# Performance work log

Measured on AMD Instinct MI355X. Metric: run time of the kernel, lower is better.

## Reference

```python
import jax, jax.numpy as jnp
import numpy as np

LN_EPS = 1e-12


def setup_inputs() -> dict:
    key = jax.random.key(0)
    k1, k2, k3, k4 = jax.random.split(key, 4)
    B, H, L, D = 2, 12, 2048, 64
    q = jax.random.normal(k1, (B, H, L, D), dtype=jnp.float32)
    k = jax.random.normal(k2, (B, H, L, D), dtype=jnp.float32)
    v = jax.random.normal(k3, (B, H, L, D), dtype=jnp.float32)
    mask = jax.random.randint(k4, (1, 1, L, L), 0, 2).astype(jnp.int32)
    gamma = jnp.ones((D,), dtype=jnp.float32)
    beta = jnp.zeros((D,), dtype=jnp.float32)
    return {"q": q, "k": k, "v": v, "mask": mask, "gamma": gamma, "beta": beta}


def reference(q, k, v, mask, gamma, beta):
    # score = q @ k^T  -> [B, H, L, L]
    score = jnp.einsum("bhqd,bhkd->bhqk", q, k)
    # masked_fill(mask == 0, -10000)
    score = jnp.where(mask == 0, jnp.float32(-10000.0), score)
    # result = score @ v -> [B, H, L, D]  (no softmax)
    result = jnp.einsum("bhqk,bhkd->bhqd", score, v)
    # layer norm over the last dim (d_tensor)
    mean = jnp.mean(result, axis=-1, keepdims=True)
    var = jnp.var(result, axis=-1, keepdims=True)
    normed = (result - mean) / jnp.sqrt(var + LN_EPS)
    return normed * gamma + beta
```

## Files before the change

### kernel.cpp

```cpp
#include <hip/hip_runtime.h>

#define SEQ 2048
#define HD 64
#define NBH 24

#define MB_OFF   0
#define MB_BYTES (32 * 32 * 512)
#define QB_OFF   (MB_OFF + MB_BYTES)
#define QK_BYTES (NBH * SEQ * HD * 2)
#define KB_OFF   (QB_OFF + QK_BYTES)
#define VT_OFF   (KB_OFF + QK_BYTES)
#define WS_NEED  ((size_t)(VT_OFF + QK_BYTES))

typedef __bf16 bfrag8 __attribute__((ext_vector_type(8)));
typedef __bf16 bf16x4 __attribute__((ext_vector_type(4)));
typedef float  floatx4 __attribute__((ext_vector_type(4)));
typedef float  floatx16 __attribute__((ext_vector_type(16)));

__device__ __forceinline__ floatx4 mfma_16x16x32(bfrag8 a, bfrag8 b, floatx4 c) {
    return __builtin_amdgcn_mfma_f32_16x16x32_bf16(a, b, c, 0, 0, 0);
}
__device__ __forceinline__ floatx16 mfma_32x32x16(bfrag8 a, bfrag8 b, floatx16 c) {
    return __builtin_amdgcn_mfma_f32_32x32x16_bf16(a, b, c, 0, 0, 0);
}
__device__ __forceinline__ void gld16(const unsigned char* g, unsigned char* l) {
    __builtin_amdgcn_global_load_lds(
        (const __attribute__((address_space(1))) unsigned int*)g,
        (__attribute__((address_space(3))) unsigned int*)l, 16, 0, 0);
}

__global__ __launch_bounds__(256)
void prep_kernel(const float* __restrict__ qp, const float* __restrict__ kp,
                 const float* __restrict__ vp, const int* __restrict__ maskp,
                 unsigned char* __restrict__ ws)
{
    __shared__ __attribute__((aligned(16))) unsigned char parena[64 * 68 * 4];
    const int t = threadIdx.x;
    const int b = blockIdx.x;

    if (b < 1536) {
        int gt  = b * 256 + t;
        int row = gt >> 3;
        int c   = gt & 7;
        const floatx4* qs = (const floatx4*)(qp + row * 64 + c * 8);
        const floatx4* ks = (const floatx4*)(kp + row * 64 + c * 8);
        floatx4 q0 = qs[0], q1 = qs[1];
        floatx4 k0 = ks[0], k1 = ks[1];
        bfrag8 qpk, kpk;
        #pragma unroll
        for (int i = 0; i < 4; ++i) {
            qpk[i] = (__bf16)q0[i]; qpk[4 + i] = (__bf16)q1[i];
            kpk[i] = (__bf16)k0[i]; kpk[4 + i] = (__bf16)k1[i];
        }
        *(bfrag8*)(ws + QB_OFF + row * 128 + c * 16) = qpk;
        *(bfrag8*)(ws + KB_OFF + row * 128 + ((c ^ (row & 7)) * 16)) = kpk;
    } else if (b < 2304) {
        int bb = b - 1536, bh = bb >> 5, kt = bb & 31;
        float* lf = (float*)parena;
        const floatx4* vg = (const floatx4*)(vp + (bh * SEQ + kt * 64) * 64);
        #pragma unroll
        for (int it = 0; it < 4; ++it) {
            int f = t + it * 256;
            int r = f >> 4, c4 = f & 15;
            floatx4 val = vg[f];
            #pragma unroll
            for (int i = 0; i < 4; ++i) lf[r * 68 + c4 * 4 + i] = val[i];
        }
        __syncthreads();
        int d = t >> 2, kseg = t & 3;
        unsigned char* tb = ws + VT_OFF + (size_t)(bh * 32 + kt) * 8192 + d * 128;
        #pragma unroll
        for (int jj = 0; jj < 2; ++jj) {
            bfrag8 pk;
            #pragma unroll
            for (int e = 0; e < 8; ++e)
                pk[e] = (__bf16)lf[(kseg * 16 + jj * 8 + e) * 68 + d];
            *(bfrag8*)(tb + (((kseg * 2 + jj) ^ (d & 7)) * 16)) = pk;
        }
    } else {
        int cc = b - 2304, qtb = cc >> 5, kt = cc & 31;
        const int w = t >> 6, lane = t & 63;
        #pragma unroll
        for (int it = 0; it < 16; ++it) {
            int rr = it * 4 + w;
            unsigned long long bl = __ballot(maskp[(qtb * 64 + rr) * SEQ + kt * 64 + lane] != 0);
            if (lane == 0)
                *(unsigned long long*)(ws + MB_OFF + (size_t)((qtb * 32 + kt) * 64 + rr) * 8) = bl;
        }
    }
}

__global__ __launch_bounds__(256, 2)
void normattn_main(const unsigned char* __restrict__ ws,
                   const float* __restrict__ gammap, const float* __restrict__ betap,
                   float* __restrict__ outp)
{
    __shared__ __attribute__((aligned(16))) unsigned char sm[65536];

    const int tid  = threadIdx.x;
    const int w    = tid >> 6;
    const int lane = tid & 63;
    const int l32  = lane & 31;
    const int hi   = lane >> 5;

    const int id   = blockIdx.x;
    const int xcd  = id & 7;
    const int s    = id >> 3;
    const int bh   = xcd * 3 + (s >> 5);
    const int qtb  = s & 31;
    const int q0   = qtb * 64;

    unsigned char* slotK = sm + w * 16384;
    unsigned char* slotV = slotK + 8192;

    const unsigned char* gKt = ws + KB_OFF + (size_t)(bh * SEQ) * 128;
    const unsigned char* gVt = ws + VT_OFF + (size_t)(bh * 32) * 8192;
    const unsigned char* gMb = ws + MB_OFF + (size_t)(qtb * 32) * 512;

    bfrag8 qb[2][4];
    #pragma unroll
    for (int qh = 0; qh < 2; ++qh)
        #pragma unroll
        for (int dstep = 0; dstep < 4; ++dstep)
            qb[qh][dstep] = *(const bfrag8*)(ws + QB_OFF +
                (size_t)(bh * SEQ + q0 + qh * 32 + l32) * 128 + dstep * 32 + hi * 16);

    floatx16 acc[2][2];
    #pragma unroll
    for (int i = 0; i < 4; ++i) acc[i >> 1][i & 1] = (floatx16)0.0f;

    auto stage = [&](int kt) {
        const unsigned char* gk = gKt + (size_t)kt * 8192 + lane * 16;
        const unsigned char* gv = gVt + (size_t)kt * 8192 + lane * 16;
        #pragma unroll
        for (int c = 0; c < 8; ++c) {
            gld16(gk + c * 1024, slotK + c * 1024);
            gld16(gv + c * 1024, slotV + c * 1024);
        }
    };
    unsigned long long mnx0, mnx1;
    auto loadmask = [&](int kt) {
        mnx0 = *(const unsigned long long*)(gMb + (size_t)kt * 512 + l32 * 8);
        mnx1 = *(const unsigned long long*)(gMb + (size_t)kt * 512 + 256 + l32 * 8);
    };

    stage(w);
    loadmask(w);

    for (int i = 0; i < 8; ++i) {
        const int kt = w + 4 * i;
        asm volatile("s_waitcnt vmcnt(0)" ::: "memory");
        const unsigned long long mr0 = mnx0, mr1 = mnx1;

        bfrag8 ka[2][4], va[2][2][2];
        #pragma unroll
        for (int kh = 0; kh < 2; ++kh)
            #pragma unroll
            for (int d = 0; d < 4; ++d)
                ka[kh][d] = *(const bfrag8*)(slotK + (kh * 32 + l32) * 128 +
                                             (((d * 2 + hi) ^ (l32 & 7)) << 4));
        #pragma unroll
        for (int dh = 0; dh < 2; ++dh)
            #pragma unroll
            for (int kh = 0; kh < 2; ++kh)
                #pragma unroll
                for (int ks = 0; ks < 2; ++ks)
                    va[dh][kh][ks] = *(const bfrag8*)(slotV + (dh * 32 + l32) * 128 +
                                                      (((kh * 4 + ks * 2 + hi) ^ (l32 & 7)) << 4));
        asm volatile("s_waitcnt lgkmcnt(0)" ::: "memory");
        if (i < 7) { stage(kt + 4); loadmask(kt + 4); }

        #pragma unroll
        for (int kh = 0; kh < 2; ++kh) {
            floatx16 st0 = (floatx16)0.0f, st1 = (floatx16)0.0f;
            #pragma unroll
            for (int d = 0; d < 4; ++d) {
                st0 = mfma_32x32x16(ka[kh][d], qb[0][d], st0);
                st1 = mfma_32x32x16(ka[kh][d], qb[1][d], st1);
            }
            #pragma unroll
            for (int qh = 0; qh < 2; ++qh) {
                const floatx16 st = qh ? st1 : st0;
                const unsigned long long mrow = qh ? mr1 : mr0;
                const unsigned bits = (unsigned)(mrow >> (kh * 32 + 4 * hi));
                unsigned u[8];
                #pragma unroll
                for (int j = 0; j < 8; ++j) {
                    const int kl0 = 2 * (j & 1) + 8 * (j >> 1);
                    float a = ((bits >> kl0) & 1u) ? st[2 * j] : -10000.0f;
                    float b = ((bits >> (kl0 + 1)) & 1u) ? st[2 * j + 1] : -10000.0f;
                    asm("v_cvt_pk_bf16_f32 %0, %1, %2" : "=v"(u[j]) : "v"(a), "v"(b));
                }
                asm("v_permlane32_swap_b32 %0, %1" : "+v"(u[0]), "+v"(u[2]));
                asm("v_permlane32_swap_b32 %0, %1" : "+v"(u[1]), "+v"(u[3]));
                asm("v_permlane32_swap_b32 %0, %1" : "+v"(u[4]), "+v"(u[6]));
                asm("v_permlane32_swap_b32 %0, %1" : "+v"(u[5]), "+v"(u[7]));
                union { unsigned int w4[4]; bfrag8 f; } c0, c1;
                c0.w4[0] = u[0]; c0.w4[1] = u[1]; c0.w4[2] = u[2]; c0.w4[3] = u[3];
                c1.w4[0] = u[4]; c1.w4[1] = u[5]; c1.w4[2] = u[6]; c1.w4[3] = u[7];

                acc[qh][0] = mfma_32x32x16(va[0][kh][0], c0.f, acc[qh][0]);
                acc[qh][0] = mfma_32x32x16(va[0][kh][1], c1.f, acc[qh][0]);
                acc[qh][1] = mfma_32x32x16(va[1][kh][0], c0.f, acc[qh][1]);
                acc[qh][1] = mfma_32x32x16(va[1][kh][1], c1.f, acc[qh][1]);
            }
        }
    }

    #pragma unroll
    for (int qh = 0; qh < 2; ++qh)
        #pragma unroll
        for (int dh = 0; dh < 2; ++dh)
            #pragma unroll
            for (int jj = 0; jj < 4; ++jj) {
                floatx4 t;
                #pragma unroll
                for (int e = 0; e < 4; ++e) t[e] = acc[qh][dh][jj * 4 + e];
                *(floatx4*)(sm + w * 16384 + (qh * 2 + dh) * 4096 + jj * 1024 + lane * 16) = t;
            }
    __syncthreads();
    if (w < 2) {
        const int qh = w;
        floatx16 o2[2];
        #pragma unroll
        for (int dh = 0; dh < 2; ++dh)
            #pragma unroll
            for (int jj = 0; jj < 4; ++jj) {
                floatx4 s4 = (floatx4)0.0f;
                #pragma unroll
                for (int ww = 0; ww < 4; ++ww) {
                    floatx4 t = *(const floatx4*)(sm + ww * 16384 + (qh * 2 + dh) * 4096 +
                                                  jj * 1024 + lane * 16);
                    #pragma unroll
                    for (int e = 0; e < 4; ++e) s4[e] += t[e];
                }
                #pragma unroll
                for (int e = 0; e < 4; ++e) o2[dh][jj * 4 + e] = s4[e];
            }
        float ss = 0.0f, ss2 = 0.0f;
        #pragma unroll
        for (int dh = 0; dh < 2; ++dh)
            #pragma unroll
            for (int r = 0; r < 16; ++r) { float x = o2[dh][r]; ss += x; ss2 += x * x; }
        ss  += __shfl_xor(ss, 32);
        ss2 += __shfl_xor(ss2, 32);
        float mean = ss * (1.0f / 64.0f);
        float var  = ss2 * (1.0f / 64.0f) - mean * mean;
        float rstd = rsqrtf(var + 1e-12f);
        float* orow = outp + (size_t)(bh * SEQ + q0 + qh * 32 + l32) * 64;
        #pragma unroll
        for (int dh = 0; dh < 2; ++dh)
            #pragma unroll
            for (int jj = 0; jj < 4; ++jj) {
                const int d0 = dh * 32 + jj * 8 + 4 * hi;
                floatx4 gg = *(const floatx4*)(gammap + d0);
                floatx4 bb = *(const floatx4*)(betap + d0);
                floatx4 o;
                #pragma unroll
                for (int e = 0; e < 4; ++e)
                    o[e] = (o2[dh][jj * 4 + e] - mean) * rstd * gg[e] + bb[e];
                *(floatx4*)(orow + d0) = o;
            }
    }
}

#define KROW 72
#define SROW 40
__global__ __launch_bounds__(256, 4)
void normattn_fallback(const float* __restrict__ qp, const float* __restrict__ kp,
                       const float* __restrict__ vp, const int* __restrict__ maskp,
                       const float* __restrict__ gammap, const float* __restrict__ betap,
                       float* __restrict__ outp)
{
    __shared__ __attribute__((aligned(16))) __bf16 sQ[64 * KROW];
    __shared__ __attribute__((aligned(16))) __bf16 sK[64 * KROW];
    __shared__ __attribute__((aligned(16))) __bf16 sV[64 * KROW];
    __shared__ __attribute__((aligned(16))) __bf16 sS[4][16 * SROW];
    __shared__ __attribute__((aligned(8)))  unsigned int sMw[64][2];

    const int tid = threadIdx.x, wave = tid >> 6, lane = tid & 63;
    const int quad = lane >> 4, l16 = lane & 15;
    const int q0 = blockIdx.x * 64, bh = blockIdx.y;
    const int base = bh * SEQ * HD;
    {
        const floatx4* qg = (const floatx4*)(qp + base + q0 * HD);
        #pragma unroll
        for (int it = 0; it < 4; ++it) {
            int idx = tid + it * 256, r = idx >> 4, c = idx & 15;
            floatx4 val = qg[idx];
            bf16x4 pk = {(__bf16)val[0], (__bf16)val[1], (__bf16)val[2], (__bf16)val[3]};
            *(bf16x4*)&sQ[r * KROW + c * 4] = pk;
        }
    }
    __syncthreads();
    bfrag8 qa0 = *(const bfrag8*)&sQ[(wave * 16 + l16) * KROW + quad * 8];
    bfrag8 qa1 = *(const bfrag8*)&sQ[(wave * 16 + l16) * KROW + quad * 8 + 32];
    floatx4 acc[4];
    #pragma unroll
    for (int i = 0; i < 4; ++i) acc[i] = (floatx4)0.0f;
    const int qrow_loc = wave * 16 + quad * 4;
    const int qrb = q0 + qrow_loc;
    for (int kb = 0; kb < SEQ; kb += 64) {
        __syncthreads();
        {
            const floatx4* kg = (const floatx4*)(kp + base + kb * HD);
            #pragma unroll
            for (int it = 0; it < 4; ++it) {
                int idx = tid + it * 256, r = idx >> 4, c = idx & 15;
                floatx4 val = kg[idx];
                bf16x4 pk = {(__bf16)val[0], (__bf16)val[1], (__bf16)val[2], (__bf16)val[3]};
                *(bf16x4*)&sK[r * KROW + c * 4] = pk;
            }
        }
        {
            int d = tid & 63;
            #pragma unroll
            for (int it = 0; it < 4; ++it) {
                int k4 = (tid >> 6) + it * 4;
                bf16x4 pk;
                #pragma unroll
                for (int i = 0; i < 4; ++i) pk[i] = (__bf16)vp[base + (kb + k4 * 4 + i) * HD + d];
                *(bf16x4*)&sV[d * KROW + k4 * 4] = pk;
            }
        }
        #pragma unroll
        for (int it = 0; it < 16; ++it) {
            int rr = it * 4 + wave;
            unsigned long long bl = __ballot(maskp[(q0 + rr) * SEQ + kb + lane] != 0);
            if (lane == 0) { sMw[rr][0] = (unsigned)bl; sMw[rr][1] = (unsigned)(bl >> 32); }
        }
        __syncthreads();
        unsigned long long mrow[4];
        #pragma unroll
        for (int r = 0; r < 4; ++r) mrow[r] = *(const unsigned long long*)&sMw[qrow_loc + r][0];
        #pragma unroll
        for (int kc = 0; kc < 64; kc += 32) {
            floatx4 s0 = (floatx4)0.0f, s1 = (floatx4)0.0f;
            bfrag8 b00 = *(const bfrag8*)&sK[(kc + l16) * KROW + quad * 8];
            bfrag8 b01 = *(const bfrag8*)&sK[(kc + l16) * KROW + quad * 8 + 32];
            bfrag8 b10 = *(const bfrag8*)&sK[(kc + 16 + l16) * KROW + quad * 8];
            bfrag8 b11 = *(const bfrag8*)&sK[(kc + 16 + l16) * KROW + quad * 8 + 32];
            s0 = mfma_16x16x32(qa0, b00, s0);
            s0 = mfma_16x16x32(qa1, b01, s0);
            s1 = mfma_16x16x32(qa0, b10, s1);
            s1 = mfma_16x16x32(qa1, b11, s1);
            #pragma unroll
            for (int r = 0; r < 4; ++r) {
                float v0 = ((mrow[r] >> (kc + l16)) & 1ull) ? s0[r] : -10000.0f;
                float v1 = ((mrow[r] >> (kc + 16 + l16)) & 1ull) ? s1[r] : -10000.0f;
                sS[wave][(quad * 4 + r) * SROW + l16] = (__bf16)v0;
                sS[wave][(quad * 4 + r) * SROW + 16 + l16] = (__bf16)v1;
            }
            asm volatile("s_waitcnt lgkmcnt(0)" ::: "memory");
            bfrag8 pa = *(const bfrag8*)&sS[wave][l16 * SROW + quad * 8];
            #pragma unroll
            for (int nt = 0; nt < 4; ++nt) {
                bfrag8 vb = *(const bfrag8*)&sV[(nt * 16 + l16) * KROW + kc + quad * 8];
                acc[nt] = mfma_16x16x32(pa, vb, acc[nt]);
            }
        }
    }
    float g[4], bt[4];
    #pragma unroll
    for (int nt = 0; nt < 4; ++nt) { g[nt] = gammap[nt * 16 + l16]; bt[nt] = betap[nt * 16 + l16]; }
    #pragma unroll
    for (int r = 0; r < 4; ++r) {
        float s = 0.0f, s2 = 0.0f;
        #pragma unroll
        for (int nt = 0; nt < 4; ++nt) { float xx = acc[nt][r]; s += xx; s2 += xx * xx; }
        #pragma unroll
        for (int off = 1; off < 16; off <<= 1) { s += __shfl_xor(s, off); s2 += __shfl_xor(s2, off); }
        float mean = s * (1.0f / 64.0f);
        float var = s2 * (1.0f / 64.0f) - mean * mean;
        float rstd = rsqrtf(var + 1e-12f);
        float* orow = outp + base + (qrb + r) * HD;
        #pragma unroll
        for (int nt = 0; nt < 4; ++nt)
            orow[nt * 16 + l16] = (acc[nt][r] - mean) * rstd * g[nt] + bt[nt];
    }
}

extern "C" void kernel_launch(void* const* d_in, const int* in_sizes, int n_in,
                              void* d_out, int out_size, void* d_ws, size_t ws_size,
                              hipStream_t stream) {
    const float* q     = (const float*)d_in[0];
    const float* k     = (const float*)d_in[1];
    const float* v     = (const float*)d_in[2];
    const int*   mask  = (const int*)d_in[3];
    const float* gamma = (const float*)d_in[4];
    const float* beta  = (const float*)d_in[5];
    float* out = (float*)d_out;

    if (ws_size >= WS_NEED) {
        unsigned char* ws = (unsigned char*)d_ws;
        prep_kernel<<<3328, 256, 0, stream>>>(q, k, v, mask, ws);
        normattn_main<<<768, 256, 0, stream>>>(ws, gamma, beta, out);
    } else {
        dim3 grid(32, NBH);
        normattn_fallback<<<grid, 256, 0, stream>>>(q, k, v, mask, gamma, beta, out);
    }
}
```

Measured before the change: 135.4 us.

## Process 128 query rows per block with Q staged in swizzled LDS

Measured after the change: 141.0 us. +4.1%, slower.

```diff
diff --git a/kernel.cpp b/kernel.cpp
--- a/kernel.cpp
+++ b/kernel.cpp
@@ -52,7 +52,7 @@
             qpk[i] = (__bf16)q0[i]; qpk[4 + i] = (__bf16)q1[i];
             kpk[i] = (__bf16)k0[i]; kpk[4 + i] = (__bf16)k1[i];
         }
-        *(bfrag8*)(ws + QB_OFF + row * 128 + c * 16) = qpk;
+        *(bfrag8*)(ws + QB_OFF + row * 128 + ((c ^ (row & 7)) * 16)) = qpk;
         *(bfrag8*)(ws + KB_OFF + row * 128 + ((c ^ (row & 7)) * 16)) = kpk;
     } else if (b < 2304) {
         int bb = b - 1536, bh = bb >> 5, kt = bb & 31;
@@ -95,7 +95,7 @@
                    const float* __restrict__ gammap, const float* __restrict__ betap,
                    float* __restrict__ outp)
 {
-    __shared__ __attribute__((aligned(16))) unsigned char sm[65536];
+    __shared__ __attribute__((aligned(16))) unsigned char sm[81920];
 
     const int tid  = threadIdx.x;
     const int w    = tid >> 6;
@@ -106,161 +106,200 @@
     const int id   = blockIdx.x;
     const int xcd  = id & 7;
     const int s    = id >> 3;
-    const int bh   = xcd * 3 + (s >> 5);
-    const int qtb  = s & 31;
-    const int q0   = qtb * 64;
+    const int bh   = xcd * 3 + (s >> 4);
+    const int qt2  = s & 15;
+    const int qbase = qt2 * 128;
 
     unsigned char* slotK = sm + w * 16384;
     unsigned char* slotV = slotK + 8192;
+    unsigned char* sQ    = sm + 65536;
 
     const unsigned char* gKt = ws + KB_OFF + (size_t)(bh * SEQ) * 128;
     const unsigned char* gVt = ws + VT_OFF + (size_t)(bh * 32) * 8192;
-    const unsigned char* gMb = ws + MB_OFF + (size_t)(qtb * 32) * 512;
-
-    bfrag8 qb[2][4];
+    const unsigned char* gQ  = ws + QB_OFF + (size_t)(bh * SEQ + qbase) * 128;
+    const unsigned char* gMb = ws + MB_OFF + (size_t)(qt2 * 2 * 32) * 512;
+
+    floatx16 acc[4][2];
     #pragma unroll
-    for (int qh = 0; qh < 2; ++qh)
-        #pragma unroll
-        for (int dstep = 0; dstep < 4; ++dstep)
-            qb[qh][dstep] = *(const bfrag8*)(ws + QB_OFF +
-                (size_t)(bh * SEQ + q0 + qh * 32 + l32) * 128 + dstep * 32 + hi * 16);
-
-    floatx16 acc[2][2];
-    #pragma unroll
-    for (int i = 0; i < 4; ++i) acc[i >> 1][i & 1] = (floatx16)0.0f;
-
-    auto stage = [&](int kt) {
+    for (int i = 0; i < 8; ++i) acc[i >> 1][i & 1] = (floatx16)0.0f;
+
+    auto stageK0 = [&](int kt) {
+        const unsigned char* gk = gKt + (size_t)kt * 8192 + lane * 16;
+        #pragma unroll
+        for (int c = 0; c < 4; ++c) gld16(gk + c * 1024, slotK + c * 1024);
+    };
+    auto stageRest = [&](int kt) {
         const unsigned char* gk = gKt + (size_t)kt * 8192 + lane * 16;
         const unsigned char* gv = gVt + (size_t)kt * 8192 + lane * 16;
         #pragma unroll
-        for (int c = 0; c < 8; ++c) {
-            gld16(gk + c * 1024, slotK + c * 1024);
-            gld16(gv + c * 1024, slotV + c * 1024);
-        }
-    };
-    unsigned long long mnx0, mnx1;
+        for (int c = 4; c < 8; ++c) gld16(gk + c * 1024, slotK + c * 1024);
+        #pragma unroll
+        for (int c = 0; c < 8; ++c) gld16(gv + c * 1024, slotV + c * 1024);
+    };
+    unsigned long long mnx[4];
     auto loadmask = [&](int kt) {
-        mnx0 = *(const unsigned long long*)(gMb + (size_t)kt * 512 + l32 * 8);
-        mnx1 = *(const unsigned long long*)(gMb + (size_t)kt * 512 + 256 + l32 * 8);
-    };
-
-    stage(w);
+        #pragma unroll
+        for (int qh = 0; qh < 4; ++qh)
+            mnx[qh] = *(const unsigned long long*)(gMb +
+                (size_t)((qh >> 1) * 32 + kt) * 512 + ((qh & 1) * 32 + l32) * 8);
+    };
+
+    auto qkpv = [&](const bfrag8 (&ka)[4], const bfrag8 (&va)[2][2], int kh, int qp,
+                    unsigned long long m0, unsigned long long m1,
+                    floatx16& a00, floatx16& a01, floatx16& a10, floatx16& a11) {
+        floatx16 st0 = (floatx16)0.0f, st1 = (floatx16)0.0f;
+        #pragma unroll
+        for (int d = 0; d < 4; ++d) {
+            const int cs = ((d * 2 + hi) ^ (l32 & 7)) << 4;
+            bfrag8 q0f = *(const bfrag8*)(sQ + (qp * 64 + l32) * 128 + cs);
+            bfrag8 q1f = *(const bfrag8*)(sQ + (qp * 64 + 32 + l32) * 128 + cs);
+            st0 = mfma_32x32x16(ka[d], q0f, st0);
+            st1 = mfma_32x32x16(ka[d], q1f, st1);
+        }
+        #pragma unroll
+        for (int qq = 0; qq < 2; ++qq) {
+            const floatx16 st = qq ? st1 : st0;
+            const unsigned long long mrow = qq ? m1 : m0;
+            const unsigned bits = (unsigned)(mrow >> (kh * 32 + 4 * hi));
+            unsigned u[8];
+            #pragma unroll
+            for (int j = 0; j < 8; ++j) {
+                const int kl0 = 2 * (j & 1) + 8 * (j >> 1);
+                float a = ((bits >> kl0) & 1u) ? st[2 * j] : -10000.0f;
+                float b = ((bits >> (kl0 + 1)) & 1u) ? st[2 * j + 1] : -10000.0f;
+                asm("v_cvt_pk_bf16_f32 %0, %1, %2" : "=v"(u[j]) : "v"(a), "v"(b));
+            }
+            asm("v_permlane32_swap_b32 %0, %1" : "+v"(u[0]), "+v"(u[2]));
+            asm("v_permlane32_swap_b32 %0, %1" : "+v"(u[1]), "+v"(u[3]));
+            asm("v_permlane32_swap_b32 %0, %1" : "+v"(u[4]), "+v"(u[6]));
+            asm("v_permlane32_swap_b32 %0, %1" : "+v"(u[5]), "+v"(u[7]));
+            union { unsigned int w4[4]; bfrag8 f; } c0, c1;
+            c0.w4[0] = u[0]; c0.w4[1] = u[1]; c0.w4[2] = u[2]; c0.w4[3] = u[3];
+            c1.w4[0] = u[4]; c1.w4[1] = u[5]; c1.w4[2] = u[6]; c1.w4[3] = u[7];
+            floatx16& ad0 = qq ? a10 : a00;
+            floatx16& ad1 = qq ? a11 : a01;
+            ad0 = mfma_32x32x16(va[0][0], c0.f, ad0);
+            ad0 = mfma_32x32x16(va[0][1], c1.f, ad0);
+            ad1 = mfma_32x32x16(va[1][0], c0.f, ad1);
+            ad1 = mfma_32x32x16(va[1][1], c1.f, ad1);
+        }
+    };
+
+    {
+        const unsigned char* gq = gQ + (size_t)(w * 32) * 128 + lane * 16;
+        unsigned char* sq = sQ + w * 4096;
+        #pragma unroll
+        for (int c = 0; c < 4; ++c) gld16(gq + c * 1024, sq + c * 1024);
+    }
+    stageK0(w);
+    stageRest(w);
     loadmask(w);
+    asm volatile("s_waitcnt vmcnt(0)" ::: "memory");
+    __builtin_amdgcn_s_barrier();
 
     for (int i = 0; i < 8; ++i) {
         const int kt = w + 4 * i;
         asm volatile("s_waitcnt vmcnt(0)" ::: "memory");
-        const unsigned long long mr0 = mnx0, mr1 = mnx1;
-
-        bfrag8 ka[2][4], va[2][2][2];
-        #pragma unroll
-        for (int kh = 0; kh < 2; ++kh)
+        const unsigned long long mr0 = mnx[0], mr1 = mnx[1], mr2 = mnx[2], mr3 = mnx[3];
+
+        {
+            bfrag8 ka[4], va[2][2];
             #pragma unroll
             for (int d = 0; d < 4; ++d)
-                ka[kh][d] = *(const bfrag8*)(slotK + (kh * 32 + l32) * 128 +
-                                             (((d * 2 + hi) ^ (l32 & 7)) << 4));
-        #pragma unroll
-        for (int dh = 0; dh < 2; ++dh)
-            #pragma unroll
-            for (int kh = 0; kh < 2; ++kh)
+                ka[d] = *(const bfrag8*)(slotK + l32 * 128 + (((d * 2 + hi) ^ (l32 & 7)) << 4));
+            #pragma unroll
+            for (int dh = 0; dh < 2; ++dh)
                 #pragma unroll
                 for (int ks = 0; ks < 2; ++ks)
-                    va[dh][kh][ks] = *(const bfrag8*)(slotV + (dh * 32 + l32) * 128 +
-                                                      (((kh * 4 + ks * 2 + hi) ^ (l32 & 7)) << 4));
-        asm volatile("s_waitcnt lgkmcnt(0)" ::: "memory");
-        if (i < 7) { stage(kt + 4); loadmask(kt + 4); }
-
-        #pragma unroll
-        for (int kh = 0; kh < 2; ++kh) {
-            floatx16 st0 = (floatx16)0.0f, st1 = (floatx16)0.0f;
-            #pragma unroll
-            for (int d = 0; d < 4; ++d) {
-                st0 = mfma_32x32x16(ka[kh][d], qb[0][d], st0);
-                st1 = mfma_32x32x16(ka[kh][d], qb[1][d], st1);
-            }
-            #pragma unroll
-            for (int qh = 0; qh < 2; ++qh) {
-                const floatx16 st = qh ? st1 : st0;
-                const unsigned long long mrow = qh ? mr1 : mr0;
-                const unsigned bits = (unsigned)(mrow >> (kh * 32 + 4 * hi));
-                unsigned u[8];
-                #pragma unroll
-                for (int j = 0; j < 8; ++j) {
-                    const int kl0 = 2 * (j & 1) + 8 * (j >> 1);
-                    float a = ((bits >> kl0) & 1u) ? st[2 * j] : -10000.0f;
-                    float b = ((bits >> (kl0 + 1)) & 1u) ? st[2 * j + 1] : -10000.0f;
-                    asm("v_cvt_pk_bf16_f32 %0, %1, %2" : "=v"(u[j]) : "v"(a), "v"(b));
+                    va[dh][ks] = *(const bfrag8*)(slotV + (dh * 32 + l32) * 128 +
+                                                  (((ks * 2 + hi) ^ (l32 & 7)) << 4));
+            asm volatile("s_waitcnt lgkmcnt(0)" ::: "memory");
+            if (i < 7) stageK0(kt + 4);
+            qkpv(ka, va, 0, 0, mr0, mr1, acc[0][0], acc[0][1], acc[1][0], acc[1][1]);
+            qkpv(ka, va, 0, 1, mr2, mr3, acc[2][0], acc[2][1], acc[3][0], acc[3][1]);
+        }
+        {
+            bfrag8 ka[4], va[2][2];
+            #pragma unroll
+            for (int d = 0; d < 4; ++d)
+                ka[d] = *(const bfrag8*)(slotK + (32 + l32) * 128 + (((d * 2 + hi) ^ (l32 & 7)) << 4));
+            #pragma unroll
+            for (int dh = 0; dh < 2; ++dh)
+                #pragma unroll
+                for (int ks = 0; ks < 2; ++ks)
+                    va[dh][ks] = *(const bfrag8*)(slotV + (dh * 32 + l32) * 128 +
+                                                  (((4 + ks * 2 + hi) ^ (l32 & 7)) << 4));
+            asm volatile("s_waitcnt lgkmcnt(0)" ::: "memory");
+            if (i < 7) { stageRest(kt + 4); loadmask(kt + 4); }
+            qkpv(ka, va, 1, 0, mr0, mr1, acc[0][0], acc[0][1], acc[1][0], acc[1][1]);
+            qkpv(ka, va, 1, 1, mr2, mr3, acc[2][0], acc[2][1], acc[3][0], acc[3][1]);
+        }
+    }
+
+    auto dumpR = [&](unsigned char* base) {
+        #pragma unroll
+        for (int qh = 0; qh < 4; ++qh)
+            #pragma unroll
+            for (int dh = 0; dh < 2; ++dh)
+                #pragma unroll
+                for (int jj = 0; jj < 4; ++jj) {
+                    floatx4 t;
+                    #pragma unroll
+                    for (int e = 0; e < 4; ++e) t[e] = acc[qh][dh][jj * 4 + e];
+                    *(floatx4*)(base + (size_t)(((qh * 2 + dh) * 4 + jj) * 1024) + lane * 16) = t;
                 }
-                asm("v_permlane32_swap_b32 %0, %1" : "+v"(u[0]), "+v"(u[2]));
-                asm("v_permlane32_swap_b32 %0, %1" : "+v"(u[1]), "+v"(u[3]));
-                asm("v_permlane32_swap_b32 %0, %1" : "+v"(u[4]), "+v"(u[6]));
-                asm("v_permlane32_swap_b32 %0, %1" : "+v"(u[5]), "+v"(u[7]));
-                union { unsigned int w4[4]; bfrag8 f; } c0, c1;
-                c0.w4[0] = u[0]; c0.w4[1] = u[1]; c0.w4[2] = u[2]; c0.w4[3] = u[3];
-                c1.w4[0] = u[4]; c1.w4[1] = u[5]; c1.w4[2] = u[6]; c1.w4[3] = u[7];
-
-                acc[qh][0] = mfma_32x32x16(va[0][kh][0], c0.f, acc[qh][0]);
-                acc[qh][0] = mfma_32x32x16(va[0][kh][1], c1.f, acc[qh][0]);
-                acc[qh][1] = mfma_32x32x16(va[1][kh][0], c0.f, acc[qh][1]);
-                acc[qh][1] = mfma_32x32x16(va[1][kh][1], c1.f, acc[qh][1]);
-            }
-        }
-    }
-
-    #pragma unroll
-    for (int qh = 0; qh < 2; ++qh)
-        #pragma unroll
-        for (int dh = 0; dh < 2; ++dh)
-            #pragma unroll
-            for (int jj = 0; jj < 4; ++jj) {
-                floatx4 t;
-                #pragma unroll
-                for (int e = 0; e < 4; ++e) t[e] = acc[qh][dh][jj * 4 + e];
-                *(floatx4*)(sm + w * 16384 + (qh * 2 + dh) * 4096 + jj * 1024 + lane * 16) = t;
-            }
+    };
+    auto addR = [&](const unsigned char* base) {
+        #pragma unroll
+        for (int qh = 0; qh < 4; ++qh)
+            #pragma unroll
+            for (int dh = 0; dh < 2; ++dh)
+                #pragma unroll
+                for (int jj = 0; jj < 4; ++jj) {
+                    floatx4 t = *(const floatx4*)(base +
+                                 (size_t)(((qh * 2 + dh) * 4 + jj) * 1024) + lane * 16);
+                    #pragma unroll
+                    for (int e = 0; e < 4; ++e) acc[qh][dh][jj * 4 + e] += t[e];
+                }
+    };
+
+    if (w == 2) dumpR(sm);
+    if (w == 3) dumpR(sm + 32768);
     __syncthreads();
-    if (w < 2) {
-        const int qh = w;
-        floatx16 o2[2];
-        #pragma unroll
-        for (int dh = 0; dh < 2; ++dh)
-            #pragma unroll
-            for (int jj = 0; jj < 4; ++jj) {
-                floatx4 s4 = (floatx4)0.0f;
-                #pragma unroll
-                for (int ww = 0; ww < 4; ++ww) {
-                    floatx4 t = *(const floatx4*)(sm + ww * 16384 + (qh * 2 + dh) * 4096 +
-                                                  jj * 1024 + lane * 16);
+    if (w == 0) addR(sm);
+    if (w == 1) addR(sm + 32768);
+    __syncthreads();
+    if (w == 1) dumpR(sm);
+    __syncthreads();
+    if (w == 0) {
+        addR(sm);
+        #pragma unroll
+        for (int qh = 0; qh < 4; ++qh) {
+            float ss = 0.0f, ss2 = 0.0f;
+            #pragma unroll
+            for (int dh = 0; dh < 2; ++dh)
+                #pragma unroll
+                for (int r = 0; r < 16; ++r) { float x = acc[qh][dh][r]; ss += x; ss2 += x * x; }
+            ss  += __shfl_xor(ss, 32);
+            ss2 += __shfl_xor(ss2, 32);
+            float mean = ss * (1.0f / 64.0f);
+            float var  = ss2 * (1.0f / 64.0f) - mean * mean;
+            float rstd = rsqrtf(var + 1e-12f);
+            float* orow = outp + (size_t)(bh * SEQ + qbase + qh * 32 + l32) * 64;
+            #pragma unroll
+            for (int dh = 0; dh < 2; ++dh)
+                #pragma unroll
+                for (int jj = 0; jj < 4; ++jj) {
+                    const int d0 = dh * 32 + jj * 8 + 4 * hi;
+                    floatx4 gg = *(const floatx4*)(gammap + d0);
+                    floatx4 bb = *(const floatx4*)(betap + d0);
+                    floatx4 o;
                     #pragma unroll
-                    for (int e = 0; e < 4; ++e) s4[e] += t[e];
+                    for (int e = 0; e < 4; ++e)
+                        o[e] = (acc[qh][dh][jj * 4 + e] - mean) * rstd * gg[e] + bb[e];
+                    *(floatx4*)(orow + d0) = o;
                 }
-                #pragma unroll
-                for (int e = 0; e < 4; ++e) o2[dh][jj * 4 + e] = s4[e];
-            }
-        float ss = 0.0f, ss2 = 0.0f;
-        #pragma unroll
-        for (int dh = 0; dh < 2; ++dh)
-            #pragma unroll
-            for (int r = 0; r < 16; ++r) { float x = o2[dh][r]; ss += x; ss2 += x * x; }
-        ss  += __shfl_xor(ss, 32);
-        ss2 += __shfl_xor(ss2, 32);
-        float mean = ss * (1.0f / 64.0f);
-        float var  = ss2 * (1.0f / 64.0f) - mean * mean;
-        float rstd = rsqrtf(var + 1e-12f);
-        float* orow = outp + (size_t)(bh * SEQ + q0 + qh * 32 + l32) * 64;
-        #pragma unroll
-        for (int dh = 0; dh < 2; ++dh)
-            #pragma unroll
-            for (int jj = 0; jj < 4; ++jj) {
-                const int d0 = dh * 32 + jj * 8 + 4 * hi;
-                floatx4 gg = *(const floatx4*)(gammap + d0);
-                floatx4 bb = *(const floatx4*)(betap + d0);
-                floatx4 o;
-                #pragma unroll
-                for (int e = 0; e < 4; ++e)
-                    o[e] = (o2[dh][jj * 4 + e] - mean) * rstd * gg[e] + bb[e];
-                *(floatx4*)(orow + d0) = o;
-            }
+        }
     }
 }
 
@@ -394,7 +433,7 @@
     if (ws_size >= WS_NEED) {
         unsigned char* ws = (unsigned char*)d_ws;
         prep_kernel<<<3328, 256, 0, stream>>>(q, k, v, mask, ws);
-        normattn_main<<<768, 256, 0, stream>>>(ws, gamma, beta, out);
+        normattn_main<<<384, 256, 0, stream>>>(ws, gamma, beta, out);
     } else {
         dim3 grid(32, NBH);
         normattn_fallback<<<grid, 256, 0, stream>>>(q, k, v, mask, gamma, beta, out);
```
